# Kernel optimization log

Hardware: AMD Instinct MI355X
Metric: run time of the kernel (lower is better)

The kernel has to match this reference:

```python
import jax, jax.numpy as jnp
import numpy as np

N, L, H, D = 4, 2048, 16, 32   # batch, seq len, heads, projection_dim
DIM = H * D                     # 512 model dim


def setup_inputs() -> dict:
    rng = jax.random.key(0)
    k1, k2, k3, k4, k5 = jax.random.split(rng, 5)
    query = jax.random.normal(k1, (N, L, DIM), dtype=jnp.float32)
    key = jax.random.normal(k2, (N, L, DIM), dtype=jnp.float32)
    scale = 0.02
    Wq = jax.random.normal(k3, (DIM, DIM), dtype=jnp.float32) * scale
    Wk = jax.random.normal(k4, (DIM, DIM), dtype=jnp.float32) * scale
    Wv = jax.random.normal(k5, (DIM, DIM), dtype=jnp.float32) * scale
    return {"query": query, "key": key, "Wq": Wq, "Wk": Wk, "Wv": Wv, "mask": 1}


def reference(query, key, Wq, Wk, Wv, mask):
    # torch Linear(bias=False): y = x @ W^T
    n, Lq, _ = query.shape
    _, Lk, _ = key.shape
    q = (query @ Wq.T).reshape(n, Lq, H, D).transpose(0, 2, 1, 3)  # (N,H,Lq,D)
    k = (key @ Wk.T).reshape(n, Lk, H, D).transpose(0, 2, 1, 3)    # (N,H,Lk,D)
    v = (key @ Wv.T).reshape(n, Lk, H, D).transpose(0, 2, 1, 3)    # (N,H,Lk,D)
    q = jax.nn.softmax(q, axis=-1)
    k = jax.nn.softmax(k, axis=-1)
    # causal branch (mask truthy): Lq*Lk > D^2*Lk, so the module takes the
    # cumsum-of-outer-products ("right") path:
    #   right = cumsum_l( k_l outer v_l );  out_l = q_l @ right_l
    kv = jnp.einsum('nhld,nhle->nhlde', k, v)   # (N,H,Lk,D,D) outer products
    S = jnp.cumsum(kv, axis=2)                  # running prefix state
    out = jnp.einsum('nhld,nhlde->nhle', q, S)  # (N,H,Lq,D)
    return out.transpose(0, 2, 1, 3).reshape(n, Lq, H * D)
```

## Files before the change

### kernel.cpp

```cpp
#include <hip/hip_runtime.h>

#define NB      4
#define L_SEQ   2048
#define H_HEADS 16
#define D32     32
#define DIM     512
#define NH      (NB * H_HEADS)
#define CHUNK   64
#define NCHUNK  (L_SEQ / CHUNK)

typedef __attribute__((ext_vector_type(8))) short bf16x8;
typedef __attribute__((ext_vector_type(4))) float f32x4;

__device__ __forceinline__ unsigned short f2bf(float x) {
    unsigned u = __float_as_uint(x);
    u += 0x7fff + ((u >> 16) & 1);
    return (unsigned short)(u >> 16);
}
__device__ __forceinline__ unsigned pack2(float lo, float hi) {
    return (unsigned)f2bf(lo) | ((unsigned)f2bf(hi) << 16);
}

__global__ __launch_bounds__(256) void gemm3_mfma_kernel(
    const float* __restrict__ query, const float* __restrict__ key,
    const float* __restrict__ Wq, const float* __restrict__ Wk,
    const float* __restrict__ Wv,
    unsigned short* __restrict__ Qs, unsigned short* __restrict__ Ks,
    unsigned short* __restrict__ Kt, unsigned short* __restrict__ Vt)
{
    const float* A; const float* W;
    const int z = blockIdx.z;
    if (z == 0)      { A = query; W = Wq; }
    else if (z == 1) { A = key;   W = Wk; }
    else             { A = key;   W = Wv; }

    __shared__ short Asm[128 * 32];
    __shared__ short Wsm[128 * 32];

    const int t    = threadIdx.x;
    const int r0   = blockIdx.y * 128;
    const int j0   = blockIdx.x * 128;
    const int w    = t >> 6;
    const int lane = t & 63;
    const int wm   = w >> 1, wn = w & 1;
    const int chunkoff = ((lane & 15) * 4 + (lane >> 4)) * 8;

    f32x4 acc[4][4] = {};

    for (int kb = 0; kb < DIM; kb += 32) {
        #pragma unroll
        for (int rep = 0; rep < 2; rep++) {
            int li  = t + rep * 256;
            int row = li >> 2, kq = li & 3;
            const float* ga = A + (size_t)(r0 + row) * DIM + kb + kq * 8;
            const float* gw = W + (size_t)(j0 + row) * DIM + kb + kq * 8;
            float4 a0 = *(const float4*)ga;
            float4 a1 = *(const float4*)(ga + 4);
            float4 w0 = *(const float4*)gw;
            float4 w1 = *(const float4*)(gw + 4);
            ((uint4*)Asm)[li] = make_uint4(pack2(a0.x, a0.y), pack2(a0.z, a0.w),
                                           pack2(a1.x, a1.y), pack2(a1.z, a1.w));
            ((uint4*)Wsm)[li] = make_uint4(pack2(w0.x, w0.y), pack2(w0.z, w0.w),
                                           pack2(w1.x, w1.y), pack2(w1.z, w1.w));
        }
        __syncthreads();

        bf16x8 af[4], bfr[4];
        #pragma unroll
        for (int i = 0; i < 4; i++)
            af[i] = *(const bf16x8*)(Asm + (wm * 4 + i) * 512 + chunkoff);
        #pragma unroll
        for (int j = 0; j < 4; j++)
            bfr[j] = *(const bf16x8*)(Wsm + (wn * 4 + j) * 512 + chunkoff);
        #pragma unroll
        for (int i = 0; i < 4; i++)
            #pragma unroll
            for (int j = 0; j < 4; j++)
                acc[i][j] = __builtin_amdgcn_mfma_f32_16x16x32_bf16(
                    af[i], bfr[j], acc[i][j], 0, 0, 0);
        __syncthreads();
    }

    if (z < 2) {
        #pragma unroll
        for (int i = 0; i < 4; i++)
            #pragma unroll
            for (int jp = 0; jp < 2; jp++)
                #pragma unroll
                for (int r = 0; r < 4; r++) {
                    float a = acc[i][2 * jp][r], b = acc[i][2 * jp + 1][r];
                    float m = fmaxf(a, b);
                    #pragma unroll
                    for (int off = 1; off < 16; off <<= 1)
                        m = fmaxf(m, __shfl_xor(m, off, 64));
                    float ea = __expf(a - m), eb = __expf(b - m);
                    float s = ea + eb;
                    #pragma unroll
                    for (int off = 1; off < 16; off <<= 1)
                        s += __shfl_xor(s, off, 64);
                    float inv = 1.0f / s;
                    acc[i][2 * jp][r]     = ea * inv;
                    acc[i][2 * jp + 1][r] = eb * inv;
                }
    }

    const int quad = lane >> 4, lc = lane & 15;
    #pragma unroll
    for (int i = 0; i < 4; i++) {
        int rbase = r0 + wm * 64 + i * 16 + quad * 4;
        #pragma unroll
        for (int r = 0; r < 4; r++) {
            int rg = rbase + r;
            int n = rg >> 11, l = rg & 2047;
            #pragma unroll
            for (int j = 0; j < 4; j++) {
                int cg = j0 + wn * 64 + j * 16 + lc;
                int h = cg >> 5, e = cg & 31;
                int nh = n * H_HEADS + h;
                unsigned short val = f2bf(acc[i][j][r]);
                if (z == 0) {
                    Qs[((size_t)nh * L_SEQ + l) * D32 + e] = val;
                } else if (z == 1) {
                    Ks[((size_t)nh * L_SEQ + l) * D32 + e] = val;
                    Kt[((size_t)nh * D32 + e) * L_SEQ + l] = val;
                } else {
                    Vt[((size_t)nh * D32 + e) * L_SEQ + l] = val;
                }
            }
        }
    }
}

__global__ __launch_bounds__(256) void chunk_kv_mfma_kernel(
    const unsigned short* __restrict__ Kt, const unsigned short* __restrict__ Vt,
    float* __restrict__ ckvT)
{
    const int nh = blockIdx.y;
    const int c  = blockIdx.x * 4 + (threadIdx.x >> 6);
    const int lane = threadIdx.x & 63;
    const int lm = lane & 15, quad = lane >> 4;

    f32x4 acc[2][2] = {};
    #pragma unroll
    for (int ch = 0; ch < 2; ch++) {
        bf16x8 aV[2], bK[2];
        #pragma unroll
        for (int mt = 0; mt < 2; mt++)
            aV[mt] = *(const bf16x8*)(Vt + ((size_t)nh * D32 + mt * 16 + lm) * L_SEQ
                                         + c * CHUNK + ch * 32 + quad * 8);
        #pragma unroll
        for (int nt = 0; nt < 2; nt++)
            bK[nt] = *(const bf16x8*)(Kt + ((size_t)nh * D32 + nt * 16 + lm) * L_SEQ
                                         + c * CHUNK + ch * 32 + quad * 8);
        #pragma unroll
        for (int mt = 0; mt < 2; mt++)
            #pragma unroll
            for (int nt = 0; nt < 2; nt++)
                acc[mt][nt] = __builtin_amdgcn_mfma_f32_16x16x32_bf16(
                    aV[mt], bK[nt], acc[mt][nt], 0, 0, 0);
    }
    #pragma unroll
    for (int mt = 0; mt < 2; mt++)
        #pragma unroll
        for (int nt = 0; nt < 2; nt++)
            #pragma unroll
            for (int r = 0; r < 4; r++) {
                int e = mt * 16 + quad * 4 + r;
                int d = nt * 16 + lm;
                ckvT[(((size_t)nh * NCHUNK + c) * 32 + e) * 32 + d] = acc[mt][nt][r];
            }
}

__global__ __launch_bounds__(256) void prefix_kernel(
    const float* __restrict__ ckvT, unsigned short* __restrict__ SpT)
{
    int nh = blockIdx.x;
    int t  = threadIdx.x;
    const float4* base = (const float4*)(ckvT + (size_t)nh * NCHUNK * 1024) + t;
    float4 vals[NCHUNK];
    #pragma unroll
    for (int c = 0; c < NCHUNK; c++) vals[c] = base[(size_t)c * 256];
    float4 acc = make_float4(0.f, 0.f, 0.f, 0.f);
    unsigned short* sp = SpT + (size_t)nh * NCHUNK * 1024 + t * 4;
    #pragma unroll
    for (int c = 0; c < NCHUNK; c++) {
        ushort4 u;
        u.x = f2bf(acc.x); u.y = f2bf(acc.y);
        u.z = f2bf(acc.z); u.w = f2bf(acc.w);
        *(ushort4*)(sp + (size_t)c * 1024) = u;
        acc.x += vals[c].x; acc.y += vals[c].y;
        acc.z += vals[c].z; acc.w += vals[c].w;
    }
}

__global__ __launch_bounds__(256) void chunk_out_mfma_kernel(
    const unsigned short* __restrict__ Qs, const unsigned short* __restrict__ Ks,
    const unsigned short* __restrict__ Vt, const unsigned short* __restrict__ SpT,
    float* __restrict__ out)
{
    const int c = blockIdx.x, nh = blockIdx.y;
    __shared__ unsigned short P[64 * 72];

    const int t = threadIdx.x, w = t >> 6, lane = t & 63;
    const int lm = lane & 15, quad = lane >> 4;

    bf16x8 aQ = *(const bf16x8*)(Qs + ((size_t)nh * L_SEQ + c * CHUNK + w * 16 + lm) * D32
                                    + quad * 8);

    #pragma unroll
    for (int j = 0; j < 4; j++) {
        f32x4 p = {};
        if (j <= w) {
            bf16x8 bK = *(const bf16x8*)(Ks + ((size_t)nh * L_SEQ + c * CHUNK + j * 16 + lm) * D32
                                            + quad * 8);
            p = __builtin_amdgcn_mfma_f32_16x16x32_bf16(aQ, bK, p, 0, 0, 0);
            if (j == w) {
                #pragma unroll
                for (int r = 0; r < 4; r++)
                    if (lm > quad * 4 + r) p[r] = 0.f;
            }
        }
        #pragma unroll
        for (int r = 0; r < 4; r++)
            P[(w * 16 + quad * 4 + r) * 72 + j * 16 + lm] = f2bf(p[r]);
    }
    __syncthreads();

    const int chains = (w < 2) ? 1 : 2;
    bf16x8 aP[2];
    for (int ch = 0; ch < chains; ch++)
        aP[ch] = *(const bf16x8*)&P[(w * 16 + lm) * 72 + ch * 32 + quad * 8];

    const int n = nh >> 4, h = nh & 15;
    #pragma unroll
    for (int nt = 0; nt < 2; nt++) {
        bf16x8 bS = *(const bf16x8*)(SpT + (((size_t)nh * NCHUNK + c) * 32 + nt * 16 + lm) * 32
                                         + quad * 8);
        f32x4 acc = {};
        acc = __builtin_amdgcn_mfma_f32_16x16x32_bf16(aQ, bS, acc, 0, 0, 0);
        for (int ch = 0; ch < chains; ch++) {
            bf16x8 bV = *(const bf16x8*)(Vt + ((size_t)nh * D32 + nt * 16 + lm) * L_SEQ
                                            + c * CHUNK + ch * 32 + quad * 8);
            acc = __builtin_amdgcn_mfma_f32_16x16x32_bf16(aP[ch], bV, acc, 0, 0, 0);
        }
        #pragma unroll
        for (int r = 0; r < 4; r++) {
            int lg = c * CHUNK + w * 16 + quad * 4 + r;
            out[((size_t)n * L_SEQ + lg) * DIM + h * D32 + nt * 16 + lm] = acc[r];
        }
    }
}

extern "C" void kernel_launch(void* const* d_in, const int* in_sizes, int n_in,
                              void* d_out, int out_size, void* d_ws, size_t ws_size,
                              hipStream_t stream)
{
    (void)in_sizes; (void)n_in; (void)out_size; (void)ws_size;
    const float* query = (const float*)d_in[0];
    const float* key   = (const float*)d_in[1];
    const float* Wq    = (const float*)d_in[2];
    const float* Wk    = (const float*)d_in[3];
    const float* Wv    = (const float*)d_in[4];
    float* out = (float*)d_out;

    const size_t SZ = (size_t)NH * L_SEQ * D32;
    unsigned short* Qs = (unsigned short*)d_ws;
    unsigned short* Ks = Qs + SZ;
    unsigned short* Kt = Ks + SZ;
    unsigned short* Vt = Kt + SZ;
    float* ckvT        = (float*)(Vt + SZ);
    unsigned short* SpT = (unsigned short*)(ckvT + (size_t)NH * NCHUNK * 1024);

    dim3 blk(256);
    gemm3_mfma_kernel<<<dim3(4, 64, 3), blk, 0, stream>>>(query, key, Wq, Wk, Wv,
                                                          Qs, Ks, Kt, Vt);
    chunk_kv_mfma_kernel<<<dim3(NCHUNK / 4, NH), blk, 0, stream>>>(Kt, Vt, ckvT);
    prefix_kernel<<<dim3(NH), blk, 0, stream>>>(ckvT, SpT);
    chunk_out_mfma_kernel<<<dim3(NCHUNK, NH), blk, 0, stream>>>(Qs, Ks, Vt, SpT, out);
}
```

Baseline: 165.3 us.

## Pre-convert inputs to bf16 and stage GEMM tiles via direct global-to-LDS loads

Adds a separate kernel that converts query, key and the three weight matrices to bf16 once. The projection GEMM then loads tiles with global_load_lds straight into shared memory instead of converting fp32 in registers. The V projection is computed transposed (Wv·keyᵀ), so its Vt stores run along the sequence, and the separate Kt buffer is dropped; the chunk kernel now gathers K with strided scalar loads from Ks. The prefix kernel loads in batches of 8 to cut register pressure. The cost is an extra launch plus a full bf16 copy written to and re-read from global memory, and the K gather in the chunk kernel is uncoalesced.

```diff
diff --git a/kernel.cpp b/kernel.cpp
--- a/kernel.cpp
+++ b/kernel.cpp
@@ -21,47 +21,70 @@
     return (unsigned)f2bf(lo) | ((unsigned)f2bf(hi) << 16);
 }
 
-__global__ __launch_bounds__(256) void gemm3_mfma_kernel(
+__device__ __forceinline__ void load_lds16(const unsigned short* g,
+                                           unsigned short* lds) {
+    __builtin_amdgcn_global_load_lds(
+        (const __attribute__((address_space(1))) unsigned int*)g,
+        (__attribute__((address_space(3))) unsigned int*)lds, 16, 0, 0);
+}
+
+#define QN  4194304
+#define WN  262144
+#define TOT (2*QN + 3*WN)
+__global__ __launch_bounds__(256) void convert_kernel(
     const float* __restrict__ query, const float* __restrict__ key,
     const float* __restrict__ Wq, const float* __restrict__ Wk,
-    const float* __restrict__ Wv,
+    const float* __restrict__ Wv, unsigned short* __restrict__ dst)
+{
+    int idx = (blockIdx.x * 256 + threadIdx.x) * 8;
+    const float* src; int off;
+    if (idx < QN)               { src = query; off = idx; }
+    else if (idx < 2*QN)        { src = key;   off = idx - QN; }
+    else if (idx < 2*QN + WN)   { src = Wq;    off = idx - 2*QN; }
+    else if (idx < 2*QN + 2*WN) { src = Wk;    off = idx - 2*QN - WN; }
+    else                        { src = Wv;    off = idx - 2*QN - 2*WN; }
+    float4 a = *(const float4*)(src + off);
+    float4 b = *(const float4*)(src + off + 4);
+    *(uint4*)(dst + idx) = make_uint4(pack2(a.x, a.y), pack2(a.z, a.w),
+                                      pack2(b.x, b.y), pack2(b.z, b.w));
+}
+
+__global__ __launch_bounds__(256) void gemm3_mfma_kernel(
+    const unsigned short* __restrict__ qb, const unsigned short* __restrict__ kb2,
+    const unsigned short* __restrict__ wqb, const unsigned short* __restrict__ wkb,
+    const unsigned short* __restrict__ wvb,
     unsigned short* __restrict__ Qs, unsigned short* __restrict__ Ks,
-    unsigned short* __restrict__ Kt, unsigned short* __restrict__ Vt)
-{
-    const float* A; const float* W;
+    unsigned short* __restrict__ Vt)
+{
     const int z = blockIdx.z;
-    if (z == 0)      { A = query; W = Wq; }
-    else if (z == 1) { A = key;   W = Wk; }
-    else             { A = key;   W = Wv; }
-
-    __shared__ short Asm[128 * 32];
-    __shared__ short Wsm[128 * 32];
+    const unsigned short *PA, *PB;
+    int m0, n0;
+    if (z == 0)      { PA = qb;  PB = wqb; m0 = blockIdx.y*128; n0 = blockIdx.x*128; }
+    else if (z == 1) { PA = kb2; PB = wkb; m0 = blockIdx.y*128; n0 = blockIdx.x*128; }
+    else             { PA = wvb; PB = kb2; m0 = blockIdx.x*128; n0 = blockIdx.y*128; }
+
+    __shared__ unsigned short Asm[128 * 32];
+    __shared__ unsigned short Bsm[128 * 32];
 
     const int t    = threadIdx.x;
-    const int r0   = blockIdx.y * 128;
-    const int j0   = blockIdx.x * 128;
     const int w    = t >> 6;
     const int lane = t & 63;
     const int wm   = w >> 1, wn = w & 1;
     const int chunkoff = ((lane & 15) * 4 + (lane >> 4)) * 8;
+    const int srow = lane >> 2, skq = lane & 3;
 
     f32x4 acc[4][4] = {};
 
     for (int kb = 0; kb < DIM; kb += 32) {
-        #pragma unroll
-        for (int rep = 0; rep < 2; rep++) {
-            int li  = t + rep * 256;
-            int row = li >> 2, kq = li & 3;
-            const float* ga = A + (size_t)(r0 + row) * DIM + kb + kq * 8;
-            const float* gw = W + (size_t)(j0 + row) * DIM + kb + kq * 8;
-            float4 a0 = *(const float4*)ga;
-            float4 a1 = *(const float4*)(ga + 4);
-            float4 w0 = *(const float4*)gw;
-            float4 w1 = *(const float4*)(gw + 4);
-            ((uint4*)Asm)[li] = make_uint4(pack2(a0.x, a0.y), pack2(a0.z, a0.w),
-                                           pack2(a1.x, a1.y), pack2(a1.z, a1.w));
-            ((uint4*)Wsm)[li] = make_uint4(pack2(w0.x, w0.y), pack2(w0.z, w0.w),
-                                           pack2(w1.x, w1.y), pack2(w1.z, w1.w));
+        {
+            const unsigned short* ga = PA + (size_t)(m0 + w*32 + srow) * DIM + kb + skq*8;
+            const unsigned short* gb = PB + (size_t)(n0 + w*32 + srow) * DIM + kb + skq*8;
+            unsigned short* la = Asm + w * 1024;
+            unsigned short* lb = Bsm + w * 1024;
+            load_lds16(ga, la);
+            load_lds16(ga + 16 * DIM, la + 512);
+            load_lds16(gb, lb);
+            load_lds16(gb + 16 * DIM, lb + 512);
         }
         __syncthreads();
 
@@ -71,7 +94,7 @@
             af[i] = *(const bf16x8*)(Asm + (wm * 4 + i) * 512 + chunkoff);
         #pragma unroll
         for (int j = 0; j < 4; j++)
-            bfr[j] = *(const bf16x8*)(Wsm + (wn * 4 + j) * 512 + chunkoff);
+            bfr[j] = *(const bf16x8*)(Bsm + (wn * 4 + j) * 512 + chunkoff);
         #pragma unroll
         for (int i = 0; i < 4; i++)
             #pragma unroll
@@ -107,24 +130,23 @@
     const int quad = lane >> 4, lc = lane & 15;
     #pragma unroll
     for (int i = 0; i < 4; i++) {
-        int rbase = r0 + wm * 64 + i * 16 + quad * 4;
+        int rbase = m0 + wm * 64 + i * 16 + quad * 4;
         #pragma unroll
         for (int r = 0; r < 4; r++) {
             int rg = rbase + r;
-            int n = rg >> 11, l = rg & 2047;
             #pragma unroll
             for (int j = 0; j < 4; j++) {
-                int cg = j0 + wn * 64 + j * 16 + lc;
-                int h = cg >> 5, e = cg & 31;
-                int nh = n * H_HEADS + h;
+                int cg = n0 + wn * 64 + j * 16 + lc;
                 unsigned short val = f2bf(acc[i][j][r]);
-                if (z == 0) {
-                    Qs[((size_t)nh * L_SEQ + l) * D32 + e] = val;
-                } else if (z == 1) {
-                    Ks[((size_t)nh * L_SEQ + l) * D32 + e] = val;
-                    Kt[((size_t)nh * D32 + e) * L_SEQ + l] = val;
+                if (z < 2) {
+                    int n = rg >> 11, l = rg & 2047;
+                    int h = cg >> 5,  e = cg & 31;
+                    unsigned short* dp = (z == 0) ? Qs : Ks;
+                    dp[(((size_t)(n * H_HEADS + h)) * L_SEQ + l) * D32 + e] = val;
                 } else {
-                    Vt[((size_t)nh * D32 + e) * L_SEQ + l] = val;
+                    int h = rg >> 5,  e = rg & 31;
+                    int n = cg >> 11, l = cg & 2047;
+                    Vt[(((size_t)(n * H_HEADS + h)) * D32 + e) * L_SEQ + l] = val;
                 }
             }
         }
@@ -132,7 +154,7 @@
 }
 
 __global__ __launch_bounds__(256) void chunk_kv_mfma_kernel(
-    const unsigned short* __restrict__ Kt, const unsigned short* __restrict__ Vt,
+    const unsigned short* __restrict__ Ks, const unsigned short* __restrict__ Vt,
     float* __restrict__ ckvT)
 {
     const int nh = blockIdx.y;
@@ -149,9 +171,13 @@
             aV[mt] = *(const bf16x8*)(Vt + ((size_t)nh * D32 + mt * 16 + lm) * L_SEQ
                                          + c * CHUNK + ch * 32 + quad * 8);
         #pragma unroll
-        for (int nt = 0; nt < 2; nt++)
-            bK[nt] = *(const bf16x8*)(Kt + ((size_t)nh * D32 + nt * 16 + lm) * L_SEQ
-                                         + c * CHUNK + ch * 32 + quad * 8);
+        for (int nt = 0; nt < 2; nt++) {
+            const unsigned short* kp = Ks
+                + ((size_t)nh * L_SEQ + c * CHUNK + ch * 32 + quad * 8) * D32
+                + nt * 16 + lm;
+            #pragma unroll
+            for (int j = 0; j < 8; j++) bK[nt][j] = (short)kp[j * D32];
+        }
         #pragma unroll
         for (int mt = 0; mt < 2; mt++)
             #pragma unroll
@@ -176,20 +202,24 @@
 {
     int nh = blockIdx.x;
     int t  = threadIdx.x;
-    const float4* base = (const float4*)(ckvT + (size_t)nh * NCHUNK * 1024) + t;
-    float4 vals[NCHUNK];
-    #pragma unroll
-    for (int c = 0; c < NCHUNK; c++) vals[c] = base[(size_t)c * 256];
+    const float* base = ckvT + (size_t)nh * NCHUNK * 1024 + t * 4;
+    unsigned short* sp = SpT + (size_t)nh * NCHUNK * 1024 + t * 4;
     float4 acc = make_float4(0.f, 0.f, 0.f, 0.f);
-    unsigned short* sp = SpT + (size_t)nh * NCHUNK * 1024 + t * 4;
-    #pragma unroll
-    for (int c = 0; c < NCHUNK; c++) {
-        ushort4 u;
-        u.x = f2bf(acc.x); u.y = f2bf(acc.y);
-        u.z = f2bf(acc.z); u.w = f2bf(acc.w);
-        *(ushort4*)(sp + (size_t)c * 1024) = u;
-        acc.x += vals[c].x; acc.y += vals[c].y;
-        acc.z += vals[c].z; acc.w += vals[c].w;
+    #pragma unroll
+    for (int cb = 0; cb < NCHUNK; cb += 8) {
+        float4 v[8];
+        #pragma unroll
+        for (int j = 0; j < 8; j++)
+            v[j] = *(const float4*)(base + (size_t)(cb + j) * 1024);
+        #pragma unroll
+        for (int j = 0; j < 8; j++) {
+            ushort4 u;
+            u.x = f2bf(acc.x); u.y = f2bf(acc.y);
+            u.z = f2bf(acc.z); u.w = f2bf(acc.w);
+            *(ushort4*)(sp + (size_t)(cb + j) * 1024) = u;
+            acc.x += v[j].x; acc.y += v[j].y;
+            acc.z += v[j].z; acc.w += v[j].w;
+        }
     }
 }
 
@@ -263,18 +293,24 @@
     const float* Wv    = (const float*)d_in[4];
     float* out = (float*)d_out;
 
+    unsigned short* bf = (unsigned short*)d_ws;
+    unsigned short* qb  = bf;
+    unsigned short* kb  = qb + QN;
+    unsigned short* wqb = kb + QN;
+    unsigned short* wkb = wqb + WN;
+    unsigned short* wvb = wkb + WN;
+    unsigned short* Qs  = wvb + WN;
     const size_t SZ = (size_t)NH * L_SEQ * D32;
-    unsigned short* Qs = (unsigned short*)d_ws;
-    unsigned short* Ks = Qs + SZ;
-    unsigned short* Kt = Ks + SZ;
-    unsigned short* Vt = Kt + SZ;
-    float* ckvT        = (float*)(Vt + SZ);
-    unsigned short* SpT = (unsigned short*)(ckvT + (size_t)NH * NCHUNK * 1024);
+    unsigned short* Ks  = Qs + SZ;
+    unsigned short* Vt  = Ks + SZ;
+    unsigned short* SpT = Vt + SZ;
+    float* ckvT = (float*)(SpT + (size_t)NH * NCHUNK * 1024);
 
     dim3 blk(256);
-    gemm3_mfma_kernel<<<dim3(4, 64, 3), blk, 0, stream>>>(query, key, Wq, Wk, Wv,
-                                                          Qs, Ks, Kt, Vt);
-    chunk_kv_mfma_kernel<<<dim3(NCHUNK / 4, NH), blk, 0, stream>>>(Kt, Vt, ckvT);
+    convert_kernel<<<dim3(TOT / (256 * 8)), blk, 0, stream>>>(query, key, Wq, Wk, Wv, qb);
+    gemm3_mfma_kernel<<<dim3(4, 64, 3), blk, 0, stream>>>(qb, kb, wqb, wkb, wvb,
+                                                          Qs, Ks, Vt);
+    chunk_kv_mfma_kernel<<<dim3(NCHUNK / 4, NH), blk, 0, stream>>>(Ks, Vt, ckvT);
     prefix_kernel<<<dim3(NH), blk, 0, stream>>>(ckvT, SpT);
     chunk_out_mfma_kernel<<<dim3(NCHUNK, NH), blk, 0, stream>>>(Qs, Ks, Vt, SpT, out);
 }
```

Measured after the change: 166.0 us. No clear change (+0.4%).
